# Kernel tuning notes

Measured on AMD Instinct MI355X. Metric: run time of the kernel, lower is better.

Reference implementation:

```python
import jax, jax.numpy as jnp
import numpy as np

D_MODEL = 768
NUM_HEADS = 12
HEAD_DIM = D_MODEL // NUM_HEADS
THETA = 10000.0
BATCH = 4
SEQ = 2048


def setup_inputs() -> dict:
    key = jax.random.key(0)
    ks = jax.random.split(key, 5)
    scale = 1.0 / np.sqrt(D_MODEL)
    x = jax.random.normal(ks[0], (BATCH, SEQ, D_MODEL), dtype=jnp.float32)
    w_q = jax.random.normal(ks[1], (D_MODEL, D_MODEL), dtype=jnp.float32) * scale
    w_k = jax.random.normal(ks[2], (D_MODEL, D_MODEL), dtype=jnp.float32) * scale
    w_v = jax.random.normal(ks[3], (D_MODEL, D_MODEL), dtype=jnp.float32) * scale
    w_o = jax.random.normal(ks[4], (D_MODEL, D_MODEL), dtype=jnp.float32) * scale
    token_positions = jnp.arange(SEQ, dtype=jnp.int32)
    return {"x": x, "w_q": w_q, "w_k": w_k, "w_v": w_v, "w_o": w_o,
            "token_positions": token_positions}


def _rope(t, positions):
    # t: [b, h, s, d]; rotate even/odd pairs with theta^(-2i/d) frequencies
    d = t.shape[-1]
    inv_freq = THETA ** (-jnp.arange(0, d, 2, dtype=jnp.float32) / d)  # [d/2]
    ang = positions.astype(jnp.float32)[:, None] * inv_freq[None, :]   # [s, d/2]
    cos, sin = jnp.cos(ang), jnp.sin(ang)
    t_even, t_odd = t[..., 0::2], t[..., 1::2]
    out_even = t_even * cos - t_odd * sin
    out_odd = t_even * sin + t_odd * cos
    return jnp.stack([out_even, out_odd], axis=-1).reshape(t.shape)


def reference(x, w_q, w_k, w_v, w_o, token_positions):
    b, s, d = x.shape
    # fused QKV projection: x @ concat(Wq, Wk, Wv).T
    w_qkv = jnp.concatenate([w_q, w_k, w_v], axis=0)  # [3d, d]
    qkv = x @ w_qkv.T                                  # [b, s, 3d]
    q, k, v = jnp.split(qkv, 3, axis=-1)
    def split_heads(t):
        return t.reshape(b, s, NUM_HEADS, HEAD_DIM).transpose(0, 2, 1, 3)  # [b,h,s,dh]
    q, k, v = split_heads(q), split_heads(k), split_heads(v)
    q = _rope(q, token_positions)
    k = _rope(k, token_positions)
    scores = jnp.einsum('bhqd,bhkd->bhqk', q, k) / np.sqrt(HEAD_DIM)  # [b,h,s,s]
    causal = jnp.tril(jnp.ones((s, s), dtype=bool))
    scores = jnp.where(causal, scores, -jnp.inf)
    attn = jax.nn.softmax(scores, axis=-1)
    out = jnp.einsum('bhqk,bhkd->bhqd', attn, v)       # [b,h,s,dh]
    out = out.transpose(0, 2, 1, 3).reshape(b, s, d)   # [b,s,d]
    return out @ w_o.T
```

## Files before the change

kernel.cpp:

```cpp
#include <hip/hip_runtime.h>
#include <hip/hip_bf16.h>
#include <math.h>

#define L2E 1.44269504088896340736f

using f32x4  = __attribute__((ext_vector_type(4))) float;
using f32x16 = __attribute__((ext_vector_type(16))) float;
using bf16x8 = __attribute__((ext_vector_type(8))) short;

static __device__ __forceinline__ float b2f(unsigned short u) {
  union { unsigned u; float f; } v; v.u = ((unsigned)u) << 16; return v.f;
}
static __device__ __forceinline__ unsigned short f2b(float f) {
  union { float f; unsigned u; } v; v.f = f;
  unsigned r = (v.u + 0x7FFFu + ((v.u >> 16) & 1u)) >> 16;
  return (unsigned short)r;
}
static __device__ __forceinline__ unsigned cvtpk(float a, float b) {
  unsigned r;
  asm("v_cvt_pk_bf16_f32 %0, %1, %2" : "=v"(r) : "v"(a), "v"(b));
  return r;
}
static __device__ __forceinline__ void plswap(unsigned& a, unsigned& b) {
#if __has_builtin(__builtin_amdgcn_permlane32_swap)
  typedef unsigned u32x2 __attribute__((ext_vector_type(2)));
  u32x2 r = __builtin_amdgcn_permlane32_swap(a, b, false, false);
  a = r[0]; b = r[1];
#else
  unsigned as = (unsigned)__shfl_xor((int)a, 32, 64);
  unsigned bs = (unsigned)__shfl_xor((int)b, 32, 64);
  bool lo = (threadIdx.x & 32) == 0;
  unsigned na = lo ? a : bs;
  unsigned nb = lo ? as : b;
  a = na; b = nb;
#endif
}

__global__ void cvt_kernel(const float* __restrict__ src,
                           unsigned short* __restrict__ dst, int n4) {
  int i = blockIdx.x * blockDim.x + threadIdx.x;
  int stride = gridDim.x * blockDim.x;
  for (; i < n4; i += stride) {
    float4 v = ((const float4*)src)[i];
    ushort4 o;
    o.x = f2b(v.x); o.y = f2b(v.y); o.z = f2b(v.z); o.w = f2b(v.w);
    ((ushort4*)dst)[i] = o;
  }
}

__global__ void wcvt_kernel(const float* __restrict__ wq, const float* __restrict__ wk,
                            const float* __restrict__ wv, unsigned short* __restrict__ dst) {
  int i = blockIdx.x * blockDim.x + threadIdx.x;
  int which = i / 147456;
  int sub = i - which * 147456;
  const float* src = which == 0 ? wq : (which == 1 ? wk : wv);
  float4 v = ((const float4*)src)[sub];
  ushort4 o;
  o.x = f2b(v.x); o.y = f2b(v.y); o.z = f2b(v.z); o.w = f2b(v.w);
  ((ushort4*)dst)[i] = o;
}

__global__ void rope_table_kernel(const int* __restrict__ pos,
                                  float2* __restrict__ tab) {
  int t = blockIdx.x * blockDim.x + threadIdx.x;
  int s = t >> 5, j = t & 31;
  double p = (double)pos[s];
  double freq = pow(10000.0, -(double)(2 * j) / 64.0);
  double ang = p * freq;
  tab[t] = make_float2((float)cos(ang), (float)sin(ang));
}

template <typename OUT>
__global__ __launch_bounds__(256) void gemm_nt(const unsigned short* __restrict__ A,
                                               const unsigned short* __restrict__ B,
                                               OUT* __restrict__ C,
                                               int M, int N, int K) {
  __shared__ unsigned short As[128 * 64];
  __shared__ unsigned short Bs[128 * 64];
  const int t = threadIdx.x;
  const int lane = t & 63;
  const int row_l = lane & 15;
  const int grp = lane >> 4;
  const int wave = t >> 6;
  const int wm = (wave >> 1) * 64;
  const int wn = (wave & 1) * 64;
  const int m0 = blockIdx.y * 128;
  const int n0 = blockIdx.x * 128;

  f32x4 acc[4][4];
#pragma unroll
  for (int i = 0; i < 4; ++i)
#pragma unroll
    for (int j = 0; j < 4; ++j) acc[i][j] = (f32x4){0.f, 0.f, 0.f, 0.f};

  const int srow = t >> 3;
  const int scolb = (t & 7) * 16;
  const size_t lda = (size_t)K * 2;
  const char* Ab = (const char*)A + (size_t)m0 * lda + scolb;
  const char* Bb = (const char*)B + (size_t)n0 * lda + scolb;

  for (int k0 = 0; k0 < K; k0 += 64) {
#pragma unroll
    for (int it = 0; it < 4; ++it) {
      int row = it * 32 + srow;
      const char* ga = Ab + (size_t)row * lda + (size_t)k0 * 2;
      const char* gb = Bb + (size_t)row * lda + (size_t)k0 * 2;
      __builtin_amdgcn_global_load_lds(
          (const __attribute__((address_space(1))) unsigned*)ga,
          (__attribute__((address_space(3))) unsigned*)((char*)As + it * 4096 + t * 16),
          16, 0, 0);
      __builtin_amdgcn_global_load_lds(
          (const __attribute__((address_space(1))) unsigned*)gb,
          (__attribute__((address_space(3))) unsigned*)((char*)Bs + it * 4096 + t * 16),
          16, 0, 0);
    }
    __syncthreads();
#pragma unroll
    for (int kk = 0; kk < 2; ++kk) {
      bf16x8 a[4], b[4];
#pragma unroll
      for (int i = 0; i < 4; ++i)
        a[i] = *(const bf16x8*)&As[(wm + 16 * i + row_l) * 64 + kk * 32 + grp * 8];
#pragma unroll
      for (int j = 0; j < 4; ++j)
        b[j] = *(const bf16x8*)&Bs[(wn + 16 * j + row_l) * 64 + kk * 32 + grp * 8];
#pragma unroll
      for (int i = 0; i < 4; ++i)
#pragma unroll
        for (int j = 0; j < 4; ++j)
          acc[i][j] = __builtin_amdgcn_mfma_f32_16x16x32_bf16(a[i], b[j], acc[i][j], 0, 0, 0);
    }
    __syncthreads();
  }
#pragma unroll
  for (int i = 0; i < 4; ++i)
#pragma unroll
    for (int j = 0; j < 4; ++j)
#pragma unroll
      for (int r = 0; r < 4; ++r) {
        int rowg = m0 + wm + 16 * i + grp * 4 + r;
        int colg = n0 + wn + 16 * j + row_l;
        float v = acc[i][j][r];
        if constexpr (sizeof(OUT) == 2) {
          C[(size_t)rowg * N + colg] = (OUT)f2b(v);
        } else {
          C[(size_t)rowg * N + colg] = v;
        }
      }
}

__global__ __launch_bounds__(256) void split_rope_kernel(
    const unsigned short* __restrict__ qkv, const float2* __restrict__ tab,
    unsigned short* __restrict__ Qo, unsigned short* __restrict__ Ko) {
  int idx = blockIdx.x * 256 + threadIdx.x;
  int d2 = idx & 31;
  int h = (idx >> 5) % 12;
  int m = idx / 384;
  int b = m >> 11, s = m & 2047;
  const unsigned short* rowp = qkv + (size_t)m * 2304;
  int c0 = h * 64 + 2 * d2;
  float qe = b2f(rowp[c0]),       qo = b2f(rowp[c0 + 1]);
  float ke = b2f(rowp[768 + c0]), ko = b2f(rowp[768 + c0 + 1]);
  float2 cs = tab[s * 32 + d2];
  float c = cs.x, sn = cs.y;
  float qre = (qe * c - qo * sn) * 0.125f;
  float qro = (qe * sn + qo * c) * 0.125f;
  float kre = ke * c - ko * sn;
  float kro = ke * sn + ko * c;
  size_t bh = (size_t)(b * 12 + h);
  size_t qoff = (bh * 2048 + s) * 64 + 2 * d2;
  ushort2 qv; qv.x = f2b(qre); qv.y = f2b(qro);
  *(ushort2*)&Qo[qoff] = qv;
  ushort2 kv; kv.x = f2b(kre); kv.y = f2b(kro);
  *(ushort2*)&Ko[qoff] = kv;
}

__global__ __launch_bounds__(256) void vtrans_kernel(
    const unsigned short* __restrict__ qkv, unsigned short* __restrict__ Vt) {
  __shared__ unsigned short T[64][72];
  const int bh = blockIdx.x;
  const int st = blockIdx.y;
  const int b = bh / 12, h = bh - b * 12;
  const int t = threadIdx.x;
  const size_t m0 = (size_t)b * 2048 + st * 64;
  const int row = t >> 2;
  const int cp = t & 3;
  const unsigned short* src = qkv + (m0 + row) * 2304 + 1536 + h * 64 + cp * 16;
  *(bf16x8*)&T[row][cp * 16]     = *(const bf16x8*)src;
  *(bf16x8*)&T[row][cp * 16 + 8] = *(const bf16x8*)(src + 8);
  __syncthreads();
  const int d = t >> 2;
  const int sp = t & 3;
  unsigned short tmp[16];
#pragma unroll
  for (int i = 0; i < 16; ++i) tmp[i] = T[sp * 16 + i][d];
  unsigned short* dst = &Vt[((size_t)bh * 64 + d) * 2048 + st * 64 + sp * 16];
  *(bf16x8*)dst       = *(bf16x8*)&tmp[0];
  *(bf16x8*)(dst + 8) = *(bf16x8*)&tmp[8];
}

__global__ __launch_bounds__(256) void attn_kernel(
    const unsigned short* __restrict__ Q, const unsigned short* __restrict__ Kc,
    const unsigned short* __restrict__ Vt, unsigned short* __restrict__ Ao) {
  __shared__ float Ob[4][32][68];
  __shared__ float Ml[4][32];
  __shared__ float Ll[4][32];
  const int lane = threadIdx.x & 63;
  const int wave = threadIdx.x >> 6;
  const int ql = lane & 31;
  const int hi = lane >> 5;
  const int bh = blockIdx.x;
  const int p = (int)gridDim.y - 1 - (int)blockIdx.y;
  const int q0 = p << 5;
  const size_t base = (size_t)bh * 2048 * 64;

  bf16x8 bq[4];
  const unsigned short* qp = &Q[base + (size_t)(q0 + ql) * 64 + hi * 8];
#pragma unroll
  for (int kk = 0; kk < 4; ++kk) bq[kk] = *(const bf16x8*)(qp + kk * 16);

  f32x16 o0, o1;
#pragma unroll
  for (int i = 0; i < 16; ++i) { o0[i] = 0.f; o1[i] = 0.f; }
  float m = -3.0e38f, lsum = 0.f;

  for (int kt = wave; kt <= p; kt += 4) {
    const int k0 = kt << 5;
    f32x16 s;
#pragma unroll
    for (int i = 0; i < 16; ++i) s[i] = 0.f;
    const unsigned short* kp = &Kc[base + (size_t)(k0 + ql) * 64 + hi * 8];
#pragma unroll
    for (int kk = 0; kk < 4; ++kk) {
      bf16x8 ak = *(const bf16x8*)(kp + kk * 16);
      s = __builtin_amdgcn_mfma_f32_32x32x16_bf16(ak, bq[kk], s, 0, 0, 0);
    }
    if (kt == p) {
#pragma unroll
      for (int r = 0; r < 16; ++r) {
        int key = k0 + (r & 3) + ((r >> 2) << 3) + (hi << 2);
        if (key > q0 + ql) s[r] = -3.0e38f;
      }
    }
    float tm = fmaxf(fmaxf(fmaxf(s[0], s[1]), fmaxf(s[2], s[3])),
                     fmaxf(fmaxf(s[4], s[5]), fmaxf(s[6], s[7])));
    tm = fmaxf(tm, fmaxf(fmaxf(fmaxf(s[8], s[9]), fmaxf(s[10], s[11])),
                         fmaxf(fmaxf(s[12], s[13]), fmaxf(s[14], s[15]))));
    tm = fmaxf(tm, __shfl_xor(tm, 32, 64));
    float nm = fmaxf(m, tm);
    float al = exp2f((m - nm) * L2E);
    m = nm;
    float mL2 = m * L2E;
    float pr[16];
    float rs = 0.f;
#pragma unroll
    for (int r = 0; r < 16; ++r) {
      float pv = exp2f(s[r] * L2E - mL2);
      pr[r] = pv;
      rs += pv;
    }
    lsum = lsum * al + rs;
    o0 *= al;
    o1 *= al;
    unsigned w0 = cvtpk(pr[0], pr[1]),   w2 = cvtpk(pr[4], pr[5]);
    unsigned w1 = cvtpk(pr[2], pr[3]),   w3 = cvtpk(pr[6], pr[7]);
    unsigned w4 = cvtpk(pr[8], pr[9]),   w6 = cvtpk(pr[12], pr[13]);
    unsigned w5 = cvtpk(pr[10], pr[11]), w7 = cvtpk(pr[14], pr[15]);
    plswap(w0, w2);
    plswap(w1, w3);
    plswap(w4, w6);
    plswap(w5, w7);
    union { unsigned u[4]; bf16x8 v; } pb0, pb1;
    pb0.u[0] = w0; pb0.u[1] = w1; pb0.u[2] = w2; pb0.u[3] = w3;
    pb1.u[0] = w4; pb1.u[1] = w5; pb1.u[2] = w6; pb1.u[3] = w7;
    const unsigned short* vp0 = &Vt[base + (size_t)ql * 2048 + k0 + hi * 8];
    const unsigned short* vp1 = vp0 + (size_t)32 * 2048;
    bf16x8 av00 = *(const bf16x8*)vp0;
    bf16x8 av01 = *(const bf16x8*)(vp0 + 16);
    bf16x8 av10 = *(const bf16x8*)vp1;
    bf16x8 av11 = *(const bf16x8*)(vp1 + 16);
    o0 = __builtin_amdgcn_mfma_f32_32x32x16_bf16(av00, pb0.v, o0, 0, 0, 0);
    o0 = __builtin_amdgcn_mfma_f32_32x32x16_bf16(av01, pb1.v, o0, 0, 0, 0);
    o1 = __builtin_amdgcn_mfma_f32_32x32x16_bf16(av10, pb0.v, o1, 0, 0, 0);
    o1 = __builtin_amdgcn_mfma_f32_32x32x16_bf16(av11, pb1.v, o1, 0, 0, 0);
  }
  float lt = lsum + __shfl_xor(lsum, 32, 64);
  if (hi == 0) { Ml[wave][ql] = m; Ll[wave][ql] = lt; }
#pragma unroll
  for (int r = 0; r < 16; ++r) {
    int d = (r & 3) + ((r >> 2) << 3) + (hi << 2);
    Ob[wave][ql][d]      = o0[r];
    Ob[wave][ql][32 + d] = o1[r];
  }
  __syncthreads();
  const int qr = (wave << 3) + (lane >> 3);
  const int db = (lane & 7) << 3;
  float m0 = Ml[0][qr], m1 = Ml[1][qr], m2 = Ml[2][qr], m3 = Ml[3][qr];
  float ms = fmaxf(fmaxf(m0, m1), fmaxf(m2, m3));
  float sc0 = exp2f((m0 - ms) * L2E);
  float sc1 = exp2f((m1 - ms) * L2E);
  float sc2 = exp2f((m2 - ms) * L2E);
  float sc3 = exp2f((m3 - ms) * L2E);
  float lstar = sc0 * Ll[0][qr] + sc1 * Ll[1][qr] + sc2 * Ll[2][qr] + sc3 * Ll[3][qr];
  float linv = 1.0f / lstar;
  unsigned short ov[8];
#pragma unroll
  for (int j = 0; j < 8; ++j) {
    float a = sc0 * Ob[0][qr][db + j] + sc1 * Ob[1][qr][db + j]
            + sc2 * Ob[2][qr][db + j] + sc3 * Ob[3][qr][db + j];
    ov[j] = f2b(a * linv);
  }
  const int b = bh / 12, h = bh - b * 12;
  *(bf16x8*)&Ao[((size_t)(b * 2048 + q0 + qr)) * 768 + h * 64 + db] = *(bf16x8*)ov;
}

extern "C" void kernel_launch(void* const* d_in, const int* in_sizes, int n_in,
                              void* d_out, int out_size, void* d_ws, size_t ws_size,
                              hipStream_t stream) {
  const float* x  = (const float*)d_in[0];
  const float* wq = (const float*)d_in[1];
  const float* wk = (const float*)d_in[2];
  const float* wv = (const float*)d_in[3];
  const float* wo = (const float*)d_in[4];
  const int* tpos = (const int*)d_in[5];
  float* out = (float*)d_out;

  char* ws = (char*)d_ws;
  unsigned short* xb   = (unsigned short*)(ws + 0);
  unsigned short* wqkv = (unsigned short*)(ws + 12582912);
  unsigned short* wob  = (unsigned short*)(ws + 16121856);
  float2*         tab  = (float2*)(ws + 17301504);
  unsigned short* qkv  = (unsigned short*)(ws + 17825792);
  unsigned short* Qb   = (unsigned short*)(ws + 55574528);
  unsigned short* Kb   = (unsigned short*)(ws + 68157440);
  unsigned short* Vtb  = (unsigned short*)(ws + 80740352);
  unsigned short* aout = xb;

  cvt_kernel<<<2048, 256, 0, stream>>>(x, xb, 8192 * 768 / 4);
  wcvt_kernel<<<1728, 256, 0, stream>>>(wq, wk, wv, wqkv);
  cvt_kernel<<<576, 256, 0, stream>>>(wo, wob, 768 * 768 / 4);
  rope_table_kernel<<<256, 256, 0, stream>>>(tpos, tab);
  gemm_nt<unsigned short><<<dim3(18, 64), 256, 0, stream>>>(xb, wqkv, qkv, 8192, 2304, 768);
  split_rope_kernel<<<12288, 256, 0, stream>>>(qkv, tab, Qb, Kb);
  vtrans_kernel<<<dim3(48, 32), 256, 0, stream>>>(qkv, Vtb);
  attn_kernel<<<dim3(48, 64), 256, 0, stream>>>(Qb, Kb, Vtb, aout);
  gemm_nt<float><<<dim3(6, 64), 256, 0, stream>>>(aout, wob, out, 8192, 768, 768);
}
```

Before: 296.4 us.

## Process 64-key tiles per wave with lazy softmax rescaling in attention

Restructures the causal attention inner loop so each wave handles 64 keys per iteration as two 32x32 score blocks. K and V loads are issued earlier so they can overlap with the MFMAs. Masking is applied only on the single diagonal tile. The online-softmax rescale of the running max, sum and output accumulators is skipped unless the tile max exceeds the running max by more than 8, and launch bounds now request 4 blocks per CU. This cuts per-iteration overhead and exp/scale work, at the cost of higher register pressure, a partly wasted masked half-tile when the query block is 64-aligned, and coarser load balancing across waves.

```diff
diff --git a/kernel.cpp b/kernel.cpp
--- a/kernel.cpp
+++ b/kernel.cpp
@@ -199,7 +199,7 @@
   *(bf16x8*)(dst + 8) = *(bf16x8*)&tmp[8];
 }
 
-__global__ __launch_bounds__(256) void attn_kernel(
+__global__ __launch_bounds__(256, 4) void attn_kernel(
     const unsigned short* __restrict__ Q, const unsigned short* __restrict__ Kc,
     const unsigned short* __restrict__ Vt, unsigned short* __restrict__ Ao) {
   __shared__ float Ob[4][32][68];
@@ -224,66 +224,98 @@
   for (int i = 0; i < 16; ++i) { o0[i] = 0.f; o1[i] = 0.f; }
   float m = -3.0e38f, lsum = 0.f;
 
-  for (int kt = wave; kt <= p; kt += 4) {
-    const int k0 = kt << 5;
-    f32x16 s;
-#pragma unroll
-    for (int i = 0; i < 16; ++i) s[i] = 0.f;
-    const unsigned short* kp = &Kc[base + (size_t)(k0 + ql) * 64 + hi * 8];
-#pragma unroll
-    for (int kk = 0; kk < 4; ++kk) {
-      bf16x8 ak = *(const bf16x8*)(kp + kk * 16);
-      s = __builtin_amdgcn_mfma_f32_32x32x16_bf16(ak, bq[kk], s, 0, 0, 0);
-    }
-    if (kt == p) {
-#pragma unroll
-      for (int r = 0; r < 16; ++r) {
-        int key = k0 + (r & 3) + ((r >> 2) << 3) + (hi << 2);
-        if (key > q0 + ql) s[r] = -3.0e38f;
-      }
-    }
-    float tm = fmaxf(fmaxf(fmaxf(s[0], s[1]), fmaxf(s[2], s[3])),
-                     fmaxf(fmaxf(s[4], s[5]), fmaxf(s[6], s[7])));
-    tm = fmaxf(tm, fmaxf(fmaxf(fmaxf(s[8], s[9]), fmaxf(s[10], s[11])),
-                         fmaxf(fmaxf(s[12], s[13]), fmaxf(s[14], s[15]))));
-    tm = fmaxf(tm, __shfl_xor(tm, 32, 64));
-    float nm = fmaxf(m, tm);
-    float al = exp2f((m - nm) * L2E);
-    m = nm;
-    float mL2 = m * L2E;
-    float pr[16];
-    float rs = 0.f;
-#pragma unroll
-    for (int r = 0; r < 16; ++r) {
-      float pv = exp2f(s[r] * L2E - mL2);
-      pr[r] = pv;
-      rs += pv;
-    }
-    lsum = lsum * al + rs;
-    o0 *= al;
-    o1 *= al;
-    unsigned w0 = cvtpk(pr[0], pr[1]),   w2 = cvtpk(pr[4], pr[5]);
-    unsigned w1 = cvtpk(pr[2], pr[3]),   w3 = cvtpk(pr[6], pr[7]);
-    unsigned w4 = cvtpk(pr[8], pr[9]),   w6 = cvtpk(pr[12], pr[13]);
-    unsigned w5 = cvtpk(pr[10], pr[11]), w7 = cvtpk(pr[14], pr[15]);
-    plswap(w0, w2);
-    plswap(w1, w3);
-    plswap(w4, w6);
-    plswap(w5, w7);
-    union { unsigned u[4]; bf16x8 v; } pb0, pb1;
-    pb0.u[0] = w0; pb0.u[1] = w1; pb0.u[2] = w2; pb0.u[3] = w3;
-    pb1.u[0] = w4; pb1.u[1] = w5; pb1.u[2] = w6; pb1.u[3] = w7;
-    const unsigned short* vp0 = &Vt[base + (size_t)ql * 2048 + k0 + hi * 8];
-    const unsigned short* vp1 = vp0 + (size_t)32 * 2048;
-    bf16x8 av00 = *(const bf16x8*)vp0;
-    bf16x8 av01 = *(const bf16x8*)(vp0 + 16);
-    bf16x8 av10 = *(const bf16x8*)vp1;
-    bf16x8 av11 = *(const bf16x8*)(vp1 + 16);
-    o0 = __builtin_amdgcn_mfma_f32_32x32x16_bf16(av00, pb0.v, o0, 0, 0, 0);
-    o0 = __builtin_amdgcn_mfma_f32_32x32x16_bf16(av01, pb1.v, o0, 0, 0, 0);
-    o1 = __builtin_amdgcn_mfma_f32_32x32x16_bf16(av10, pb0.v, o1, 0, 0, 0);
-    o1 = __builtin_amdgcn_mfma_f32_32x32x16_bf16(av11, pb1.v, o1, 0, 0, 0);
-  }
+  const unsigned short* kbase  = &Kc[base + (size_t)ql * 64 + hi * 8];
+  const unsigned short* vbase0 = &Vt[base + (size_t)ql * 2048 + hi * 8];
+  const unsigned short* vbase1 = vbase0 + (size_t)32 * 2048;
+  const int nfull = q0 >> 6;
+
+#define BODY64(K0, DOMASK)                                                     \
+  {                                                                            \
+    const int k0_ = (K0);                                                      \
+    const unsigned short* kp = kbase + (size_t)k0_ * 64;                       \
+    bf16x8 ak[4];                                                              \
+    f32x16 slo, shi;                                                           \
+    _Pragma("unroll") for (int i = 0; i < 16; ++i) { slo[i] = 0.f; shi[i] = 0.f; } \
+    _Pragma("unroll") for (int kk = 0; kk < 4; ++kk)                           \
+        ak[kk] = *(const bf16x8*)(kp + kk * 16);                               \
+    _Pragma("unroll") for (int kk = 0; kk < 4; ++kk)                           \
+        slo = __builtin_amdgcn_mfma_f32_32x32x16_bf16(ak[kk], bq[kk], slo, 0, 0, 0); \
+    _Pragma("unroll") for (int kk = 0; kk < 4; ++kk)                           \
+        ak[kk] = *(const bf16x8*)(kp + 32 * 64 + kk * 16);                     \
+                           \
+    const unsigned short* vp0 = vbase0 + k0_;                                  \
+    bf16x8 av0[4];                                                             \
+    _Pragma("unroll") for (int c = 0; c < 4; ++c)                              \
+        av0[c] = *(const bf16x8*)(vp0 + c * 16);                               \
+    _Pragma("unroll") for (int kk = 0; kk < 4; ++kk)                           \
+        shi = __builtin_amdgcn_mfma_f32_32x32x16_bf16(ak[kk], bq[kk], shi, 0, 0, 0); \
+    if (DOMASK) {                                                              \
+      _Pragma("unroll") for (int r = 0; r < 16; ++r) {                         \
+        int key = k0_ + (r & 3) + ((r >> 2) << 3) + (hi << 2);                 \
+        if (key > q0 + ql)      slo[r] = -3.0e38f;                             \
+        if (key + 32 > q0 + ql) shi[r] = -3.0e38f;                             \
+      }                                                                        \
+    }                                                                          \
+    float t0 = fmaxf(fmaxf(fmaxf(slo[0], slo[1]), fmaxf(slo[2], slo[3])),     \
+                     fmaxf(fmaxf(slo[4], slo[5]), fmaxf(slo[6], slo[7])));    \
+    float t1 = fmaxf(fmaxf(fmaxf(slo[8], slo[9]), fmaxf(slo[10], slo[11])),   \
+                     fmaxf(fmaxf(slo[12], slo[13]), fmaxf(slo[14], slo[15]))); \
+    float t2 = fmaxf(fmaxf(fmaxf(shi[0], shi[1]), fmaxf(shi[2], shi[3])),     \
+                     fmaxf(fmaxf(shi[4], shi[5]), fmaxf(shi[6], shi[7])));    \
+    float t3 = fmaxf(fmaxf(fmaxf(shi[8], shi[9]), fmaxf(shi[10], shi[11])),   \
+                     fmaxf(fmaxf(shi[12], shi[13]), fmaxf(shi[14], shi[15]))); \
+    float tm = fmaxf(fmaxf(t0, t1), fmaxf(t2, t3));                            \
+    tm = fmaxf(tm, __shfl_xor(tm, 32, 64));                                    \
+    if (!__all(tm <= m + 8.0f)) {                                              \
+      float nm = fmaxf(m, tm);                                                 \
+      float al = exp2f((m - nm) * L2E);                                        \
+      m = nm;                                                                  \
+      lsum *= al;                                                              \
+      o0 *= al;                                                                \
+      o1 *= al;                                                                \
+    }                                                                          \
+    float mL2 = m * L2E;                                                       \
+    float rs = 0.f;                                                            \
+    _Pragma("unroll") for (int r = 0; r < 16; ++r) {                           \
+      slo[r] = exp2f(slo[r] * L2E - mL2); rs += slo[r];                        \
+    }                                                                          \
+    _Pragma("unroll") for (int r = 0; r < 16; ++r) {                           \
+      shi[r] = exp2f(shi[r] * L2E - mL2); rs += shi[r];                        \
+    }                                                                          \
+    lsum += rs;                                                                \
+    unsigned w0 = cvtpk(slo[0], slo[1]),   w2 = cvtpk(slo[4], slo[5]);         \
+    unsigned w1 = cvtpk(slo[2], slo[3]),   w3 = cvtpk(slo[6], slo[7]);         \
+    unsigned w4 = cvtpk(slo[8], slo[9]),   w6 = cvtpk(slo[12], slo[13]);       \
+    unsigned w5 = cvtpk(slo[10], slo[11]), w7 = cvtpk(slo[14], slo[15]);       \
+    plswap(w0, w2); plswap(w1, w3); plswap(w4, w6); plswap(w5, w7);            \
+    union { unsigned u[4]; bf16x8 v; } pb0, pb1, pb2, pb3;                     \
+    pb0.u[0] = w0; pb0.u[1] = w1; pb0.u[2] = w2; pb0.u[3] = w3;                \
+    pb1.u[0] = w4; pb1.u[1] = w5; pb1.u[2] = w6; pb1.u[3] = w7;                \
+    unsigned x0 = cvtpk(shi[0], shi[1]),   x2 = cvtpk(shi[4], shi[5]);         \
+    unsigned x1 = cvtpk(shi[2], shi[3]),   x3 = cvtpk(shi[6], shi[7]);         \
+    unsigned x4 = cvtpk(shi[8], shi[9]),   x6 = cvtpk(shi[12], shi[13]);       \
+    unsigned x5 = cvtpk(shi[10], shi[11]), x7 = cvtpk(shi[14], shi[15]);       \
+    plswap(x0, x2); plswap(x1, x3); plswap(x4, x6); plswap(x5, x7);            \
+    pb2.u[0] = x0; pb2.u[1] = x1; pb2.u[2] = x2; pb2.u[3] = x3;                \
+    pb3.u[0] = x4; pb3.u[1] = x5; pb3.u[2] = x6; pb3.u[3] = x7;                \
+    const unsigned short* vp1 = vbase1 + k0_;                                  \
+    bf16x8 av1[4];                                                             \
+    _Pragma("unroll") for (int c = 0; c < 4; ++c)                              \
+        av1[c] = *(const bf16x8*)(vp1 + c * 16);                               \
+    o0 = __builtin_amdgcn_mfma_f32_32x32x16_bf16(av0[0], pb0.v, o0, 0, 0, 0);  \
+    o0 = __builtin_amdgcn_mfma_f32_32x32x16_bf16(av0[1], pb1.v, o0, 0, 0, 0);  \
+    o0 = __builtin_amdgcn_mfma_f32_32x32x16_bf16(av0[2], pb2.v, o0, 0, 0, 0);  \
+    o0 = __builtin_amdgcn_mfma_f32_32x32x16_bf16(av0[3], pb3.v, o0, 0, 0, 0);  \
+    o1 = __builtin_amdgcn_mfma_f32_32x32x16_bf16(av1[0], pb0.v, o1, 0, 0, 0);  \
+    o1 = __builtin_amdgcn_mfma_f32_32x32x16_bf16(av1[1], pb1.v, o1, 0, 0, 0);  \
+    o1 = __builtin_amdgcn_mfma_f32_32x32x16_bf16(av1[2], pb2.v, o1, 0, 0, 0);  \
+    o1 = __builtin_amdgcn_mfma_f32_32x32x16_bf16(av1[3], pb3.v, o1, 0, 0, 0);  \
+  }
+
+  for (int t = wave; t < nfull; t += 4) BODY64(t << 6, false)
+  if (wave == (nfull & 3)) BODY64(nfull << 6, true)
+#undef BODY64
+
   float lt = lsum + __shfl_xor(lsum, 32, 64);
   if (hi == 0) { Ml[wave][ql] = m; Ll[wave][ql] = lt; }
 #pragma unroll
```

After: 293.1 us. About the same (-1.1%).

## Process 64-key tiles per wave with lazy rescaling and bf16 partial-output merge

Applied to the files above, without the earlier changes.

The attention loop now handles 64 keys per iteration (two 32x32 score MFMAs) instead of 32, so each softmax rescale and V accumulation covers more keys and K/V loads are issued earlier to overlap with MFMA work. The online-softmax rescale is skipped unless the new max exceeds the running max by more than a threshold, which cuts exp and multiply work. Per-wave partial outputs go to shared memory as packed bf16 rather than fp32, shrinking LDS use, and launch bounds request 6 blocks per CU for occupancy. The risks are extra register pressure from the wider tile, rounding error from bf16 partials, and possible overflow if the threshold is ever exceeded in a bad way.

```diff
diff --git a/kernel.cpp b/kernel.cpp
--- a/kernel.cpp
+++ b/kernel.cpp
@@ -199,10 +199,10 @@
   *(bf16x8*)(dst + 8) = *(bf16x8*)&tmp[8];
 }
 
-__global__ __launch_bounds__(256) void attn_kernel(
+__global__ __launch_bounds__(256, 6) void attn_kernel(
     const unsigned short* __restrict__ Q, const unsigned short* __restrict__ Kc,
     const unsigned short* __restrict__ Vt, unsigned short* __restrict__ Ao) {
-  __shared__ float Ob[4][32][68];
+  __shared__ unsigned Obp[4][32][36];
   __shared__ float Ml[4][32];
   __shared__ float Ll[4][32];
   const int lane = threadIdx.x & 63;
@@ -224,77 +224,107 @@
   for (int i = 0; i < 16; ++i) { o0[i] = 0.f; o1[i] = 0.f; }
   float m = -3.0e38f, lsum = 0.f;
 
-  for (int kt = wave; kt <= p; kt += 4) {
-    const int k0 = kt << 5;
-    f32x16 s;
-#pragma unroll
-    for (int i = 0; i < 16; ++i) s[i] = 0.f;
-    const unsigned short* kp = &Kc[base + (size_t)(k0 + ql) * 64 + hi * 8];
-#pragma unroll
-    for (int kk = 0; kk < 4; ++kk) {
-      bf16x8 ak = *(const bf16x8*)(kp + kk * 16);
-      s = __builtin_amdgcn_mfma_f32_32x32x16_bf16(ak, bq[kk], s, 0, 0, 0);
-    }
-    if (kt == p) {
+  const unsigned short* kbase  = &Kc[base + (size_t)ql * 64 + hi * 8];
+  const unsigned short* vbase0 = &Vt[base + (size_t)ql * 2048 + hi * 8];
+  const unsigned short* vbase1 = vbase0 + (size_t)32 * 2048;
+  const int nfull = q0 >> 6;
+
+  for (int t = wave; t <= nfull; t += 4) {
+    const int k0 = t << 6;
+    const bool domask = (t == nfull);
+    const unsigned short* kp = kbase + (size_t)k0 * 64;
+    bf16x8 ak[4];
+    f32x16 slo, shi;
+#pragma unroll
+    for (int i = 0; i < 16; ++i) { slo[i] = 0.f; shi[i] = 0.f; }
+#pragma unroll
+    for (int kk = 0; kk < 4; ++kk) ak[kk] = *(const bf16x8*)(kp + kk * 16);
+#pragma unroll
+    for (int kk = 0; kk < 4; ++kk)
+      slo = __builtin_amdgcn_mfma_f32_32x32x16_bf16(ak[kk], bq[kk], slo, 0, 0, 0);
+#pragma unroll
+    for (int kk = 0; kk < 4; ++kk) ak[kk] = *(const bf16x8*)(kp + 32 * 64 + kk * 16);
+    const unsigned short* vp0 = vbase0 + k0;
+    bf16x8 av0[4];
+#pragma unroll
+    for (int c = 0; c < 4; ++c) av0[c] = *(const bf16x8*)(vp0 + c * 16);
+#pragma unroll
+    for (int kk = 0; kk < 4; ++kk)
+      shi = __builtin_amdgcn_mfma_f32_32x32x16_bf16(ak[kk], bq[kk], shi, 0, 0, 0);
+    if (domask) {
 #pragma unroll
       for (int r = 0; r < 16; ++r) {
         int key = k0 + (r & 3) + ((r >> 2) << 3) + (hi << 2);
-        if (key > q0 + ql) s[r] = -3.0e38f;
+        if (key > q0 + ql)      slo[r] = -3.0e38f;
+        if (key + 32 > q0 + ql) shi[r] = -3.0e38f;
       }
     }
-    float tm = fmaxf(fmaxf(fmaxf(s[0], s[1]), fmaxf(s[2], s[3])),
-                     fmaxf(fmaxf(s[4], s[5]), fmaxf(s[6], s[7])));
-    tm = fmaxf(tm, fmaxf(fmaxf(fmaxf(s[8], s[9]), fmaxf(s[10], s[11])),
-                         fmaxf(fmaxf(s[12], s[13]), fmaxf(s[14], s[15]))));
+    float t0 = fmaxf(fmaxf(fmaxf(slo[0], slo[1]), fmaxf(slo[2], slo[3])),
+                     fmaxf(fmaxf(slo[4], slo[5]), fmaxf(slo[6], slo[7])));
+    float t1 = fmaxf(fmaxf(fmaxf(slo[8], slo[9]), fmaxf(slo[10], slo[11])),
+                     fmaxf(fmaxf(slo[12], slo[13]), fmaxf(slo[14], slo[15])));
+    float t2 = fmaxf(fmaxf(fmaxf(shi[0], shi[1]), fmaxf(shi[2], shi[3])),
+                     fmaxf(fmaxf(shi[4], shi[5]), fmaxf(shi[6], shi[7])));
+    float t3 = fmaxf(fmaxf(fmaxf(shi[8], shi[9]), fmaxf(shi[10], shi[11])),
+                     fmaxf(fmaxf(shi[12], shi[13]), fmaxf(shi[14], shi[15])));
+    float tm = fmaxf(fmaxf(t0, t1), fmaxf(t2, t3));
     tm = fmaxf(tm, __shfl_xor(tm, 32, 64));
-    float nm = fmaxf(m, tm);
-    float al = exp2f((m - nm) * L2E);
-    m = nm;
+    if (!__all(tm <= m + 8.0f)) {
+      float nm = fmaxf(m, tm);
+      float al = exp2f((m - nm) * L2E);
+      m = nm;
+      lsum *= al;
+      o0 *= al;
+      o1 *= al;
+    }
     float mL2 = m * L2E;
-    float pr[16];
     float rs = 0.f;
 #pragma unroll
-    for (int r = 0; r < 16; ++r) {
-      float pv = exp2f(s[r] * L2E - mL2);
-      pr[r] = pv;
-      rs += pv;
-    }
-    lsum = lsum * al + rs;
-    o0 *= al;
-    o1 *= al;
-    unsigned w0 = cvtpk(pr[0], pr[1]),   w2 = cvtpk(pr[4], pr[5]);
-    unsigned w1 = cvtpk(pr[2], pr[3]),   w3 = cvtpk(pr[6], pr[7]);
-    unsigned w4 = cvtpk(pr[8], pr[9]),   w6 = cvtpk(pr[12], pr[13]);
-    unsigned w5 = cvtpk(pr[10], pr[11]), w7 = cvtpk(pr[14], pr[15]);
-    plswap(w0, w2);
-    plswap(w1, w3);
-    plswap(w4, w6);
-    plswap(w5, w7);
-    union { unsigned u[4]; bf16x8 v; } pb0, pb1;
+    for (int r = 0; r < 16; ++r) { slo[r] = exp2f(slo[r] * L2E - mL2); rs += slo[r]; }
+#pragma unroll
+    for (int r = 0; r < 16; ++r) { shi[r] = exp2f(shi[r] * L2E - mL2); rs += shi[r]; }
+    lsum += rs;
+    unsigned w0 = cvtpk(slo[0], slo[1]),   w2 = cvtpk(slo[4], slo[5]);
+    unsigned w1 = cvtpk(slo[2], slo[3]),   w3 = cvtpk(slo[6], slo[7]);
+    unsigned w4 = cvtpk(slo[8], slo[9]),   w6 = cvtpk(slo[12], slo[13]);
+    unsigned w5 = cvtpk(slo[10], slo[11]), w7 = cvtpk(slo[14], slo[15]);
+    plswap(w0, w2); plswap(w1, w3); plswap(w4, w6); plswap(w5, w7);
+    union { unsigned u[4]; bf16x8 v; } pb0, pb1, pb2, pb3;
     pb0.u[0] = w0; pb0.u[1] = w1; pb0.u[2] = w2; pb0.u[3] = w3;
     pb1.u[0] = w4; pb1.u[1] = w5; pb1.u[2] = w6; pb1.u[3] = w7;
-    const unsigned short* vp0 = &Vt[base + (size_t)ql * 2048 + k0 + hi * 8];
-    const unsigned short* vp1 = vp0 + (size_t)32 * 2048;
-    bf16x8 av00 = *(const bf16x8*)vp0;
-    bf16x8 av01 = *(const bf16x8*)(vp0 + 16);
-    bf16x8 av10 = *(const bf16x8*)vp1;
-    bf16x8 av11 = *(const bf16x8*)(vp1 + 16);
-    o0 = __builtin_amdgcn_mfma_f32_32x32x16_bf16(av00, pb0.v, o0, 0, 0, 0);
-    o0 = __builtin_amdgcn_mfma_f32_32x32x16_bf16(av01, pb1.v, o0, 0, 0, 0);
-    o1 = __builtin_amdgcn_mfma_f32_32x32x16_bf16(av10, pb0.v, o1, 0, 0, 0);
-    o1 = __builtin_amdgcn_mfma_f32_32x32x16_bf16(av11, pb1.v, o1, 0, 0, 0);
-  }
+    unsigned x0 = cvtpk(shi[0], shi[1]),   x2 = cvtpk(shi[4], shi[5]);
+    unsigned x1 = cvtpk(shi[2], shi[3]),   x3 = cvtpk(shi[6], shi[7]);
+    unsigned x4 = cvtpk(shi[8], shi[9]),   x6 = cvtpk(shi[12], shi[13]);
+    unsigned x5 = cvtpk(shi[10], shi[11]), x7 = cvtpk(shi[14], shi[15]);
+    plswap(x0, x2); plswap(x1, x3); plswap(x4, x6); plswap(x5, x7);
+    pb2.u[0] = x0; pb2.u[1] = x1; pb2.u[2] = x2; pb2.u[3] = x3;
+    pb3.u[0] = x4; pb3.u[1] = x5; pb3.u[2] = x6; pb3.u[3] = x7;
+    const unsigned short* vp1 = vbase1 + k0;
+    bf16x8 av1[4];
+#pragma unroll
+    for (int c = 0; c < 4; ++c) av1[c] = *(const bf16x8*)(vp1 + c * 16);
+    o0 = __builtin_amdgcn_mfma_f32_32x32x16_bf16(av0[0], pb0.v, o0, 0, 0, 0);
+    o0 = __builtin_amdgcn_mfma_f32_32x32x16_bf16(av0[1], pb1.v, o0, 0, 0, 0);
+    o0 = __builtin_amdgcn_mfma_f32_32x32x16_bf16(av0[2], pb2.v, o0, 0, 0, 0);
+    o0 = __builtin_amdgcn_mfma_f32_32x32x16_bf16(av0[3], pb3.v, o0, 0, 0, 0);
+    o1 = __builtin_amdgcn_mfma_f32_32x32x16_bf16(av1[0], pb0.v, o1, 0, 0, 0);
+    o1 = __builtin_amdgcn_mfma_f32_32x32x16_bf16(av1[1], pb1.v, o1, 0, 0, 0);
+    o1 = __builtin_amdgcn_mfma_f32_32x32x16_bf16(av1[2], pb2.v, o1, 0, 0, 0);
+    o1 = __builtin_amdgcn_mfma_f32_32x32x16_bf16(av1[3], pb3.v, o1, 0, 0, 0);
+  }
+
   float lt = lsum + __shfl_xor(lsum, 32, 64);
   if (hi == 0) { Ml[wave][ql] = m; Ll[wave][ql] = lt; }
 #pragma unroll
-  for (int r = 0; r < 16; ++r) {
-    int d = (r & 3) + ((r >> 2) << 3) + (hi << 2);
-    Ob[wave][ql][d]      = o0[r];
-    Ob[wave][ql][32 + d] = o1[r];
+  for (int j = 0; j < 4; ++j) {
+    Obp[wave][ql][4 * j + 2 * hi]          = cvtpk(o0[4 * j],     o0[4 * j + 1]);
+    Obp[wave][ql][4 * j + 2 * hi + 1]      = cvtpk(o0[4 * j + 2], o0[4 * j + 3]);
+    Obp[wave][ql][16 + 4 * j + 2 * hi]     = cvtpk(o1[4 * j],     o1[4 * j + 1]);
+    Obp[wave][ql][16 + 4 * j + 2 * hi + 1] = cvtpk(o1[4 * j + 2], o1[4 * j + 3]);
   }
   __syncthreads();
   const int qr = (wave << 3) + (lane >> 3);
-  const int db = (lane & 7) << 3;
+  const int l7 = lane & 7;
   float m0 = Ml[0][qr], m1 = Ml[1][qr], m2 = Ml[2][qr], m3 = Ml[3][qr];
   float ms = fmaxf(fmaxf(m0, m1), fmaxf(m2, m3));
   float sc0 = exp2f((m0 - ms) * L2E);
@@ -305,13 +335,20 @@
   float linv = 1.0f / lstar;
   unsigned short ov[8];
 #pragma unroll
-  for (int j = 0; j < 8; ++j) {
-    float a = sc0 * Ob[0][qr][db + j] + sc1 * Ob[1][qr][db + j]
-            + sc2 * Ob[2][qr][db + j] + sc3 * Ob[3][qr][db + j];
-    ov[j] = f2b(a * linv);
+  for (int c = 0; c < 4; ++c) {
+    unsigned u0 = Obp[0][qr][l7 * 4 + c];
+    unsigned u1 = Obp[1][qr][l7 * 4 + c];
+    unsigned u2 = Obp[2][qr][l7 * 4 + c];
+    unsigned u3 = Obp[3][qr][l7 * 4 + c];
+    float lo = sc0 * b2f((unsigned short)u0) + sc1 * b2f((unsigned short)u1)
+             + sc2 * b2f((unsigned short)u2) + sc3 * b2f((unsigned short)u3);
+    float hv = sc0 * b2f((unsigned short)(u0 >> 16)) + sc1 * b2f((unsigned short)(u1 >> 16))
+             + sc2 * b2f((unsigned short)(u2 >> 16)) + sc3 * b2f((unsigned short)(u3 >> 16));
+    ov[2 * c]     = f2b(lo * linv);
+    ov[2 * c + 1] = f2b(hv * linv);
   }
   const int b = bh / 12, h = bh - b * 12;
-  *(bf16x8*)&Ao[((size_t)(b * 2048 + q0 + qr)) * 768 + h * 64 + db] = *(bf16x8*)ov;
+  *(bf16x8*)&Ao[((size_t)(b * 2048 + q0 + qr)) * 768 + h * 64 + l7 * 8] = *(bf16x8*)ov;
 }
 
 extern "C" void kernel_launch(void* const* d_in, const int* in_sizes, int n_in,
```

New measurement: 456.9 us. +54.1%, slower.
